# Optimization experiments

Hardware: AMD Instinct MI355X
Metric: run time of the kernel (lower is better)

## Reference

```python
import jax, jax.numpy as jnp
import numpy as np
import math

SPARSITY = 0.5
EPS = 1e-5


def _quant(x, bit, after_relu):
    # mirrors torch quantize_per_tensor math; straight-through (torch mutates x.data)
    def q(x):
        mx, mn = x.max(), x.min()
        scale = (mx - mn) / (2 ** bit - 1)
        if after_relu:
            ir = jnp.clip(jnp.round(x / scale), 0.0, 2 ** bit - 1)
            return ir * scale
        zp_min = jnp.floor(mn / scale)
        return (jnp.round((x - mn) / scale) + zp_min) * scale
    return x + jax.lax.stop_gradient(q(x) - x)


def _subnet(scores, k):
    # GetSubnet: top-k mask of |scores| with straight-through gradient
    s = jnp.abs(scores)
    flat = s.ravel()
    j = int((1.0 - k) * flat.size)
    order = jnp.argsort(flat)
    mask = jnp.zeros_like(flat).at[order[j:]].set(1.0).reshape(s.shape)
    return jax.lax.stop_gradient(mask - s) + s


def _scale(hw_one, fan_in):
    std = math.sqrt(2.0) / math.sqrt(fan_in * 0.5)
    return hw_one.mean() / std


def _blend_w(scores, sign, hw_one, hw_zero):
    m = _subnet(scores, SPARSITY)
    return sign * (hw_one[0] * m + hw_zero[0] * (1.0 - m))


def _conv(x, w):
    return jax.lax.conv_general_dilated(x, w, (1, 1), 'VALID',
                                        dimension_numbers=('NCHW', 'OIHW', 'NCHW'))


def _maxpool2(x):
    return jax.lax.reduce_window(x, -jnp.inf, jax.lax.max,
                                 (1, 1, 2, 2), (1, 1, 2, 2), 'VALID')


def _bn(x):
    m = x.mean((0, 2, 3), keepdims=True)
    v = x.var((0, 2, 3), keepdims=True)
    return (x - m) / jnp.sqrt(v + EPS)


def setup_inputs() -> dict:
    key = jax.random.key(0)
    ks = jax.random.split(key, 16)
    B = 4096
    shapes = {
        '1': (64, 1, 3, 3),
        '2': (16, 64, 3, 3),
        '3': (128, 400),
        '4': (10, 128),
    }
    inp = {'x': jax.random.normal(ks[0], (B, 1, 28, 28), dtype=jnp.float32)}
    i = 1
    for name, shp in shapes.items():
        inp['scores' + name] = jax.random.normal(ks[i], shp, dtype=jnp.float32); i += 1
        inp['sign' + name] = jnp.sign(jax.random.normal(ks[i], shp, dtype=jnp.float32)); i += 1
        inp['hw' + name + '_one'] = jax.random.uniform(ks[i], (1,) + shp, dtype=jnp.float32); i += 1
        # hw_zero: small "off" conductances
        inp['hw' + name + '_zero'] = 0.05 * jax.random.uniform(jax.random.fold_in(ks[i], 1), (1,) + shp, dtype=jnp.float32)
    inp['qb'] = 8
    return inp


def reference(x, scores1, sign1, hw1_one, hw1_zero,
              scores2, sign2, hw2_one, hw2_zero,
              scores3, sign3, hw3_one, hw3_zero,
              scores4, sign4, hw4_one, hw4_zero, qb):
    x = _maxpool2(x)
    x = _quant(x, qb, False)
    # conv1 (fan_in = 1*3*3 = 9)
    w1 = _blend_w(scores1, sign1, hw1_one, hw1_zero)
    x = _conv(x, w1) / _scale(hw1_one, 9)
    x = jax.nn.relu(_bn(x))
    x = _quant(x, qb, True)
    # conv2 (fan_in = 64*9 = 576)
    w2 = _blend_w(scores2, sign2, hw2_one, hw2_zero)
    x = _conv(x, w2) / _scale(hw2_one, 576)
    x = _maxpool2(x)
    x = jax.nn.relu(_bn(x))
    x = _quant(x, qb, True)
    x = x.reshape(x.shape[0], -1)  # [B, 400]
    # fc1 (fan_in = 400)
    w3 = _blend_w(scores3, sign3, hw3_one, hw3_zero)
    x = (x @ w3.T) / _scale(hw3_one, 400)
    x = jax.nn.relu(x)
    x = _quant(x, qb, True)
    # fc2 (fan_in = 128)
    w4 = _blend_w(scores4, sign4, hw4_one, hw4_zero)
    x = (x @ w4.T) / _scale(hw4_one, 128)
    return jax.nn.log_softmax(x, axis=1)
```

## Files before the change

### kernel.cpp

```cpp
#include <hip/hip_runtime.h>
#include <hip/hip_bf16.h>
#include <math.h>

#define DEV __device__ __forceinline__

constexpr int BATCH = 4096;
constexpr int NBA = 512;
constexpr int NBB = 512;
constexpr int NBC = 4096;
constexpr int NBE = 256;
constexpr int NBW = 16;

constexpr size_t OFF_POOLED = 0;
constexpr size_t OFF_Y2P = OFF_POOLED + (size_t)BATCH*196;
constexpr size_t OFF_ST1 = OFF_Y2P;
constexpr size_t OFF_H3  = OFF_Y2P + (size_t)BATCH*400;
constexpr size_t OFF_ST2 = OFF_H3;
constexpr size_t OFF_W2  = OFF_H3 + (size_t)BATCH*128;
constexpr size_t OFF_W3  = OFF_W2 + 9216;
constexpr size_t OFF_W4  = OFF_W3 + 51200;
constexpr size_t OFF_WSC = OFF_W4 + 1280;
constexpr size_t OFF_BN1 = OFF_WSC + 4;
constexpr size_t OFF_BN2 = OFF_BN1 + 256;
constexpr size_t OFF_GMM = OFF_BN2 + 64;
constexpr size_t OFF_ONS = OFF_GMM + 8;
constexpr size_t OFF_T   = OFF_ONS + 16;
constexpr size_t OFF_MMA = OFF_T + 4;
constexpr size_t OFF_HIST= OFF_MMA + 1024;
constexpr size_t OFF_W1M = OFF_HIST + 32768;
constexpr size_t OFF_SEL = OFF_W1M + 2048;
constexpr size_t OFF_H2G = OFF_SEL + 8;
constexpr size_t OFF_H3G = OFF_H2G + 4096;

typedef __attribute__((ext_vector_type(8))) short bf16x8;
typedef __attribute__((ext_vector_type(4))) float f32x4;

struct InPtrs {
  const float* x;
  const float* sc[4];
  const float* sg[4];
  const float* on[4];
  const float* ze[4];
  const int* qb;
};

__constant__ const int KW_L[16]  ={0,1,1,2,2,2,2,2,2,2,2,2,2,2,2,3};
__constant__ const int KW_S[16]  ={0,0,1,0,1,2,3,4,5,6,7,8,9,10,11,0};
__constant__ const int KW_NB[4]  ={1,2,12,1};
__constant__ const int KW_N[4]   ={576,9216,51200,1280};
__constant__ const int KW_FAN[4] ={9,576,400,128};
__constant__ const int KW_BW0[4] ={0,1,3,15};
__constant__ const int KW_BW1[4] ={1,3,15,16};

DEV unsigned fenc(float f){ unsigned u=__float_as_uint(f); return (u&0x80000000u)? ~u : (u|0x80000000u); }
DEV float fdec(unsigned e){ return __uint_as_float((e&0x80000000u)? (e&0x7fffffffu) : ~e); }
DEV unsigned short f2bf(float f){ unsigned u=__float_as_uint(f); return (unsigned short)((u + 0x7fffu + ((u>>16)&1u))>>16); }

DEV float blk_sum(float v, float* red, int t){
  red[t]=v; __syncthreads();
  for (int s=128;s>0;s>>=1){ if(t<s) red[t]+=red[t+s]; __syncthreads(); }
  float r=red[0]; __syncthreads();
  return r;
}
DEV float blk_min(float v, float* red, int t){
  red[t]=v; __syncthreads();
  for (int s=128;s>0;s>>=1){ if(t<s) red[t]=fminf(red[t],red[t+s]); __syncthreads(); }
  float r=red[0]; __syncthreads();
  return r;
}
DEV float blk_max(float v, float* red, int t){
  red[t]=v; __syncthreads();
  for (int s=128;s>0;s>>=1){ if(t<s) red[t]=fmaxf(red[t],red[t+s]); __syncthreads(); }
  float r=red[0]; __syncthreads();
  return r;
}

DEV int2 find256(const int* hist, int nbins, int kk, int t, int* suf, int* sh2){
  const int G=nbins>>8;
  const int lo=t*G;
  int g=0;
  for (int b=0;b<G;++b) g+=hist[lo+b];
  suf[t]=g; __syncthreads();
  for (int s=1;s<256;s<<=1){
    int add=(t+s<256)?suf[t+s]:0;
    __syncthreads();
    suf[t]+=add;
    __syncthreads();
  }
  const int S=suf[t];
  const int Snext=(t<255)?suf[t+1]:0;
  if (S>=kk && Snext<kk){
    int c2=Snext;
    for (int b=lo+G-1;b>=lo;--b){
      c2+=hist[b];
      if (c2>=kk){ sh2[0]=b; sh2[1]=kk-(c2-hist[b]); break; }
    }
  }
  __syncthreads();
  int2 r=make_int2(sh2[0],sh2[1]);
  __syncthreads();
  return r;
}

DEV void build_patq(unsigned* PATQ, const unsigned short* qxs, int t){
  for (int pos=t; pos<144; pos+=256){
    int py=(pos*171)>>11;
    int px=pos-py*12;
    const unsigned short* q0=qxs+py*16+px;
    unsigned e0=q0[0],  e1=q0[1],  e2=q0[2];
    unsigned e3=q0[16], e4=q0[17], e5=q0[18];
    unsigned e6=q0[32], e7=q0[33], e8=q0[34];
    *(uint4*)(PATQ+pos*4)      =make_uint4(e0|(e1<<16), e2|(e3<<16), e4|(e5<<16), e6|(e7<<16));
    *(uint4*)(PATQ+(144+pos)*4)=make_uint4(e8, 0u, 0u, 0u);
  }
}

__global__ __launch_bounds__(256) void ka_kernel(InPtrs in, float* __restrict__ ws){
  const int t=threadIdx.x, blk=blockIdx.x;
  __shared__ int h[2048];
  __shared__ float red[256];
  if (blk<NBA){
    if (blk==0){
      unsigned* Z=(unsigned*)(ws+OFF_H2G);
      for (int i=t;i<8192;i+=256) Z[i]=0u;
    }
    const float* x=in.x;
    float* pooled=ws+OFF_POOLED;
    float lmn=3.4e38f, lmx=-3.4e38f;
    if (t<196){
      const int oy=(t*2341)>>15;
      const int ox=t-oy*14;
      const float* xb=x+(size_t)blk*8*784+oy*56+ox*2;
      #pragma unroll
      for (int im=0; im<8; ++im){
        const float* px=xb+im*784;
        float m=fmaxf(fmaxf(px[0],px[1]),fmaxf(px[28],px[29]));
        pooled[(size_t)(blk*8+im)*196+t]=m;
        lmn=fminf(lmn,m); lmx=fmaxf(lmx,m);
      }
    }
    float bmn=blk_min(lmn,red,t);
    float bmx=blk_max(lmx,red,t);
    if (t==0){ ws[OFF_MMA+blk*2]=bmn; ws[OFF_MMA+blk*2+1]=bmx; }
  } else {
    const int bw=blk-NBA;
    const int L=KW_L[bw], s=KW_S[bw], nb=KW_NB[L];
    const int n4=KW_N[L]>>2;
    const int lo=(int)(((long long)n4*s)/nb), hi=(int)(((long long)n4*(s+1))/nb);
    const float4* sc4=(const float4*)in.sc[L];
    const float4* on4=(const float4*)in.on[L];
    for (int i=t;i<2048;i+=256) h[i]=0;
    __syncthreads();
    float onsum=0.f;
    for (int i=lo+t;i<hi;i+=256){
      float4 v=sc4[i];
      atomicAdd(&h[(__float_as_uint(v.x)&0x7fffffffu)>>20],1);
      atomicAdd(&h[(__float_as_uint(v.y)&0x7fffffffu)>>20],1);
      atomicAdd(&h[(__float_as_uint(v.z)&0x7fffffffu)>>20],1);
      atomicAdd(&h[(__float_as_uint(v.w)&0x7fffffffu)>>20],1);
      float4 o=on4[i];
      onsum+=(o.x+o.y)+(o.z+o.w);
    }
    __syncthreads();
    unsigned* GH=(unsigned*)(ws+OFF_HIST);
    for (int i=t;i<2048;i+=256) GH[bw*2048+i]=(unsigned)h[i];
    float S=blk_sum(onsum,red,t);
    if (t==0) ws[OFF_ONS+bw]=S;
  }
}

__global__ __launch_bounds__(256) void kwp2_kernel(InPtrs in, float* __restrict__ ws){
  const int t=threadIdx.x, bw=blockIdx.x;
  __shared__ int hist[2048];
  __shared__ int suf[256];
  __shared__ int sh2[2];
  __shared__ float redm[256], redx[256];
  const int L=KW_L[bw], s=KW_S[bw], nb=KW_NB[L];
  const int n4=KW_N[L]>>2;
  const int lo=(int)(((long long)n4*s)/nb), hi=(int)(((long long)n4*(s+1))/nb);
  if (bw==0){
    float a0=ws[OFF_MMA+2*t],       a1=ws[OFF_MMA+2*(t+256)];
    float b0v=ws[OFF_MMA+2*t+1],    b1v=ws[OFF_MMA+2*(t+256)+1];
    redm[t]=fminf(a0,a1); redx[t]=fmaxf(b0v,b1v);
    __syncthreads();
    for (int st=128;st>0;st>>=1){
      if (t<st){ redm[t]=fminf(redm[t],redm[t+st]); redx[t]=fmaxf(redx[t],redx[t+st]); }
      __syncthreads();
    }
    unsigned* U=(unsigned*)(ws+OFF_GMM);
    if (t==0){ U[0]=fenc(redm[0]); U[1]=fenc(redx[0]); }
    if (t>=2 && t<8) U[t]=(t&1)? 0u : 0xFFFFFFFFu;
    __syncthreads();
  }
  if (bw==15){
    unsigned* z=(unsigned*)(ws+OFF_W1M);
    for (int i=t;i<2048;i+=256) z[i]=0u;
  }
  const unsigned* GH=(const unsigned*)(ws+OFF_HIST);
  for (int i=t;i<2048;i+=256){
    int sm=0;
    for (int b2=KW_BW0[L]; b2<KW_BW1[L]; ++b2) sm+=(int)GH[b2*2048+i];
    hist[i]=sm;
  }
  __syncthreads();
  int2 f1=find256(hist,2048,KW_N[L]>>1,t,suf,sh2);
  const unsigned b0=(unsigned)f1.x;
  if (s==0 && t==0){
    unsigned* SEL=(unsigned*)(ws+OFF_SEL);
    SEL[L*2]=(unsigned)f1.x; SEL[L*2+1]=(unsigned)f1.y;
  }
  const float4* sc4=(const float4*)in.sc[L];
  unsigned* GH2=(unsigned*)(ws+OFF_H2G)+L*1024;
  for (int i=lo+t;i<hi;i+=256){
    float4 v=sc4[i];
    unsigned ux=__float_as_uint(v.x)&0x7fffffffu;
    unsigned uy=__float_as_uint(v.y)&0x7fffffffu;
    unsigned uz=__float_as_uint(v.z)&0x7fffffffu;
    unsigned uw=__float_as_uint(v.w)&0x7fffffffu;
    if ((ux>>20)==b0) atomicAdd(&GH2[(ux>>10)&1023u],1u);
    if ((uy>>20)==b0) atomicAdd(&GH2[(uy>>10)&1023u],1u);
    if ((uz>>20)==b0) atomicAdd(&GH2[(uz>>10)&1023u],1u);
    if ((uw>>20)==b0) atomicAdd(&GH2[(uw>>10)&1023u],1u);
  }
}

__global__ __launch_bounds__(256) void kwp3_kernel(InPtrs in, float* __restrict__ ws){
  const int t=threadIdx.x, bw=blockIdx.x;
  const int L=KW_L[bw], s=KW_S[bw], nb=KW_NB[L];
  const int n4=KW_N[L]>>2;
  const int lo=(int)(((long long)n4*s)/nb), hi=(int)(((long long)n4*(s+1))/nb);
  const unsigned* SEL=(const unsigned*)(ws+OFF_SEL);
  const unsigned b0=SEL[L*2]; const int r1=(int)SEL[L*2+1];
  __shared__ int hist[1024];
  __shared__ int suf[256];
  __shared__ int sh2[2];
  const unsigned* GH2=(const unsigned*)(ws+OFF_H2G)+L*1024;
  for (int i=t;i<1024;i+=256) hist[i]=(int)GH2[i];
  __syncthreads();
  int2 f2=find256(hist,1024,r1,t,suf,sh2);
  const unsigned pre=(b0<<10)|(unsigned)f2.x;
  const float4* sc4=(const float4*)in.sc[L];
  unsigned* GH3=(unsigned*)(ws+OFF_H3G)+L*1024;
  for (int i=lo+t;i<hi;i+=256){
    float4 v=sc4[i];
    unsigned ux=__float_as_uint(v.x)&0x7fffffffu;
    unsigned uy=__float_as_uint(v.y)&0x7fffffffu;
    unsigned uz=__float_as_uint(v.z)&0x7fffffffu;
    unsigned uw=__float_as_uint(v.w)&0x7fffffffu;
    if ((ux>>10)==pre) atomicAdd(&GH3[ux&1023u],1u);
    if ((uy>>10)==pre) atomicAdd(&GH3[uy&1023u],1u);
    if ((uz>>10)==pre) atomicAdd(&GH3[uz&1023u],1u);
    if ((uw>>10)==pre) atomicAdd(&GH3[uw&1023u],1u);
  }
}

__global__ __launch_bounds__(256) void kw3_kernel(InPtrs in, float* __restrict__ ws){
  const int t=threadIdx.x, bw=blockIdx.x;
  const int L=KW_L[bw], s=KW_S[bw], nb=KW_NB[L];
  const int n4=KW_N[L]>>2;
  const int lo=(int)(((long long)n4*s)/nb), hi=(int)(((long long)n4*(s+1))/nb);
  const unsigned* SEL=(const unsigned*)(ws+OFF_SEL);
  const unsigned b0=SEL[L*2]; const int r1=(int)SEL[L*2+1];
  __shared__ int hist[1024];
  __shared__ int suf[256];
  __shared__ int sh2[2];
  const unsigned* GH2=(const unsigned*)(ws+OFF_H2G)+L*1024;
  for (int i=t;i<1024;i+=256) hist[i]=(int)GH2[i];
  __syncthreads();
  int2 f2=find256(hist,1024,r1,t,suf,sh2);
  const unsigned pre=(b0<<10)|(unsigned)f2.x;
  const int r2=f2.y;
  __syncthreads();
  const unsigned* GH3=(const unsigned*)(ws+OFF_H3G)+L*1024;
  for (int i=t;i<1024;i+=256) hist[i]=(int)GH3[i];
  __syncthreads();
  int2 f3=find256(hist,1024,r2,t,suf,sh2);
  const unsigned T=(pre<<10)|(unsigned)f3.x;
  if (s==0 && t==0){
    float os=0.f;
    for (int b=KW_BW0[L]; b<KW_BW1[L]; ++b) os+=ws[OFF_ONS+b];
    ws[OFF_WSC+L]=(os/(float)KW_N[L])*sqrtf((float)KW_FAN[L])*0.5f;
  }
  const float4* sc4=(const float4*)in.sc[L];
  const float4* sg4=(const float4*)in.sg[L];
  const float4* on4=(const float4*)in.on[L];
  const float4* ze4=(const float4*)in.ze[L];
  float* wout=ws+OFF_W4;
  unsigned* W3Fu=(unsigned*)(ws+OFF_W3);
  unsigned short* W1F=(unsigned short*)(ws+OFF_W1M);
  unsigned short* W2F=(unsigned short*)(ws+OFF_W2);
  for (int i4=lo+t;i4<hi;i4+=256){
    float4 sv4=sc4[i4], g=sg4[i4], o=on4[i4], z=ze4[i4];
    float sv[4]={sv4.x,sv4.y,sv4.z,sv4.w}, gv[4]={g.x,g.y,g.z,g.w};
    float ov[4]={o.x,o.y,o.z,o.w}, zv[4]={z.x,z.y,z.z,z.w};
    #pragma unroll
    for (int j=0;j<4;++j){
      int i=i4*4+j;
      unsigned u=__float_as_uint(sv[j])&0x7fffffffu;
      float w=gv[j]*((u>=T)? ov[j] : zv[j]);
      if (L==0){
        int oc=i/9; int k=i-oc*9;
        int ocT=oc>>4, ocL=oc&15, quad=k>>3, kj=k&7;
        unsigned short hb=f2bf(w);
        float lo2=w-__uint_as_float((unsigned)hb<<16);
        W1F[((((ocT*2+0)*4+quad)*16+ocL)<<3)+kj]=hb;
        W1F[((((ocT*2+1)*4+quad)*16+ocL)<<3)+kj]=f2bf(lo2);
      } else if (L==1){
        int oc=i/576; int r=i-oc*576; int ic=r/9; int kp=r-ic*9;
        int ss=ic>>5, rem=ic&31, quad=rem>>3, kj=rem&7;
        unsigned short hb=f2bf(w);
        float lo2=w-__uint_as_float((unsigned)hb<<16);
        W2F[(((((kp*2+ss)*2+0)*4+quad)*16+oc)<<3)+kj]=hb;
        W2F[(((((kp*2+ss)*2+1)*4+quad)*16+oc)<<3)+kj]=f2bf(lo2);
      } else if (L==2){
        int oc=i/400; int kk=i-oc*400;
        unsigned short hb=f2bf(w);
        float lo2=w-__uint_as_float((unsigned)hb<<16);
        unsigned short lb=f2bf(lo2);
        int ct=oc>>4, l15=oc&15;
        unsigned idx=((unsigned)((kk>>4)*8+ct)*64u + (unsigned)(((kk>>2)&3)*16+l15))*4u + (unsigned)(kk&3);
        W3Fu[idx]=(unsigned)hb | ((unsigned)lb<<16);
      } else {
        wout[i]=w;
      }
    }
  }
}

__global__ __launch_bounds__(256) void kb_kernel(InPtrs in, const float* __restrict__ wsr, float* __restrict__ wsw){
  const int t=threadIdx.x, blk=blockIdx.x;
  __shared__ unsigned short qxs[256];
  __shared__ __align__(16) unsigned PAT[2304];
  __shared__ float xw[1024];
  const float* pooled=wsr+OFF_POOLED;
  const unsigned* U=(const unsigned*)(wsr+OFF_GMM);
  const float mn0=fdec(U[0]);
  const float mx0=fdec(U[1]);
  const float lvf=(float)((1<<in.qb[0])-1);
  const float s0=(mx0-mn0)/lvf, inv_s0=1.0f/s0, zp0=floorf(mn0/s0);
  const float sv=s0/wsr[OFF_WSC+0];
  const int w=t>>6, lane=t&63, l15=lane&15, quad=lane>>4;
  const unsigned short* W1F=(const unsigned short*)(wsr+OFF_W1M);
  bf16x8 bh[4], bl[4];
  #pragma unroll
  for (int ocT=0; ocT<4; ++ocT){
    bh[ocT]=*(const bf16x8*)(W1F+(((ocT*2+0)*64+lane)<<3));
    bl[ocT]=*(const bf16x8*)(W1F+(((ocT*2+1)*64+lane)<<3));
  }
  for (int i=1152+t; i<2304; i+=256) PAT[i]=0u;
  float sum[4], sq[4], mn[4], mx[4];
  #pragma unroll
  for (int i=0;i<4;++i){ sum[i]=0.f; sq[i]=0.f; mn[i]=3.4e38f; mx[i]=-3.4e38f; }
  for (int img=0; img<8; ++img){
    if (t<224){
      int row=t>>4, col=t&15;
      float q=0.f;
      if (col<14){ float xx=pooled[(size_t)(blk*8+img)*196+row*14+col]; q=rintf((xx-mn0)*inv_s0)+zp0; }
      qxs[t]=(unsigned short)(__float_as_uint(q)>>16);
    }
    __syncthreads();
    build_patq(PAT,qxs,t);
    __syncthreads();
    const unsigned short* PATu=(const unsigned short*)PAT;
    #pragma unroll
    for (int ocT=0; ocT<4; ++ocT){
      for (int tl=w; tl<9; tl+=4){
        bf16x8 a=*(const bf16x8*)(PATu+((quad*144+tl*16+l15)<<3));
        f32x4 acc=(f32x4){0.f,0.f,0.f,0.f};
        acc=__builtin_amdgcn_mfma_f32_16x16x32_bf16(a,bh[ocT],acc,0,0,0);
        acc=__builtin_amdgcn_mfma_f32_16x16x32_bf16(a,bl[ocT],acc,0,0,0);
        #pragma unroll
        for (int r=0;r<4;++r){
          float v=acc[r];
          sum[ocT]+=v; sq[ocT]=fmaf(v,v,sq[ocT]);
          mn[ocT]=fminf(mn[ocT],v); mx[ocT]=fmaxf(mx[ocT],v);
        }
      }
    }
    __syncthreads();
  }
  #pragma unroll
  for (int ocT=0; ocT<4; ++ocT){
    float s=sum[ocT], q2=sq[ocT], a=mn[ocT], b=mx[ocT];
    #pragma unroll
    for (int d=16;d<64;d<<=1){
      s+=__shfl_xor(s,d);
      q2+=__shfl_xor(q2,d);
      a=fminf(a,__shfl_xor(a,d));
      b=fmaxf(b,__shfl_xor(b,d));
    }
    if (quad==0){
      float* p=xw+((w*4+ocT)*16+l15)*4;
      p[0]=s; p[1]=q2; p[2]=a; p[3]=b;
    }
  }
  __syncthreads();
  if (t<64){
    float s=0.f,q2=0.f,a=3.4e38f,b=-3.4e38f;
    #pragma unroll
    for (int w2=0;w2<4;++w2){
      const float* p=xw+((w2*4+(t>>4))*16+(t&15))*4;
      s+=p[0]; q2+=p[1]; a=fminf(a,p[2]); b=fmaxf(b,p[3]);
    }
    float* p=wsw+OFF_ST1+((size_t)t*NBB+blk)*4;
    p[0]=s*sv; p[1]=q2*sv*sv; p[2]=a*sv; p[3]=b*sv;
  }
}

__global__ __launch_bounds__(256) void kstat_kernel(const float* __restrict__ wsr, float* __restrict__ wsw,
                                                    unsigned long long inoff, int nparts, float Nf,
                                                    unsigned long long outoff, int mmslot){
  const int c=blockIdx.x, t=threadIdx.x;
  __shared__ float red[256];
  const float* p=wsr+inoff+(size_t)c*nparts*4;
  float sum=0.f,sq=0.f,mn=3.4e38f,mx=-3.4e38f;
  for (int i=t;i<nparts;i+=256){
    sum+=p[i*4]; sq+=p[i*4+1];
    mn=fminf(mn,p[i*4+2]); mx=fmaxf(mx,p[i*4+3]);
  }
  float S=blk_sum(sum,red,t);
  float Q=blk_sum(sq,red,t);
  float MN=blk_min(mn,red,t);
  float MX=blk_max(mx,red,t);
  if (t==0){
    float mean=S/Nf;
    float var=fmaxf(Q/Nf-mean*mean,0.f);
    float sd=sqrtf(var+1e-5f);
    float* o=wsw+outoff+c*4;
    float tmn=(MN-mean)/sd, tmx=(MX-mean)/sd;
    o[0]=mean; o[1]=sd; o[2]=tmn; o[3]=tmx;
    unsigned* U=(unsigned*)(wsw+OFF_GMM);
    atomicMin(&U[mmslot],fenc(tmn));
    atomicMax(&U[mmslot+1],fenc(tmx));
  }
}

__global__ __launch_bounds__(256) void kc_kernel(InPtrs in, const float* __restrict__ wsr, float* __restrict__ wsw){
  const int t=threadIdx.x, blk=blockIdx.x;
  __shared__ unsigned short qxs[256];
  __shared__ __align__(16) unsigned PATBUF[3328];
  __shared__ __align__(16) unsigned short actA[144*88];
  __shared__ float sA2[64], sB2[64];
  unsigned* PAT=PATBUF;
  float (*c2sP)[16][104]=(float(*)[16][104])PATBUF;
  const float* pooled=wsr+OFF_POOLED;
  const unsigned* U=(const unsigned*)(wsr+OFF_GMM);
  const float mn0=fdec(U[0]);
  const float mx0=fdec(U[1]);
  const float rmn=fdec(U[2]);
  const float rmx=fdec(U[3]);
  const float lvf=(float)((1<<in.qb[0])-1);
  const float s0=(mx0-mn0)/lvf, inv_s0=1.0f/s0, zp0=floorf(mn0/s0);
  const float s1w=wsr[OFF_WSC+0], s2w=wsr[OFF_WSC+1];
  const float s2=(fmaxf(rmx,0.f)-fmaxf(rmn,0.f))/lvf;
  const float inv_s2=1.0f/s2;
  const float g2=s2/s2w;
  if (t<64){
    float m=wsr[OFF_BN1+t*4], sd=wsr[OFF_BN1+t*4+1];
    sA2[t]=s0/(s1w*sd)*inv_s2;
    sB2[t]=(-m/sd)*inv_s2;
  }
  if (t<224){
    int row=t>>4, col=t&15;
    float q=0.f;
    if (col<14){ float xx=pooled[(size_t)blk*196+row*14+col]; q=rintf((xx-mn0)*inv_s0)+zp0; }
    qxs[t]=(unsigned short)(__float_as_uint(q)>>16);
  }
  for (int i=1152+t; i<2304; i+=256) PAT[i]=0u;
  __syncthreads();
  build_patq(PAT,qxs,t);
  __syncthreads();
  const int w=t>>6, lane=t&63;
  const int l15=lane&15, quad=lane>>4;
  {
    const unsigned short* W1F=(const unsigned short*)(wsr+OFF_W1M);
    const unsigned short* PATu=(const unsigned short*)PAT;
    #pragma unroll
    for (int ocT=0; ocT<4; ++ocT){
      bf16x8 bh=*(const bf16x8*)(W1F+(((ocT*2+0)*64+lane)<<3));
      bf16x8 bl=*(const bf16x8*)(W1F+(((ocT*2+1)*64+lane)<<3));
      const int oc0=ocT*16+quad*4;
      const float a20=sA2[oc0],   b20=sB2[oc0];
      const float a21=sA2[oc0+1], b21=sB2[oc0+1];
      const float a22=sA2[oc0+2], b22=sB2[oc0+2];
      const float a23=sA2[oc0+3], b23=sB2[oc0+3];
      for (int tl=w; tl<9; tl+=4){
        bf16x8 a=*(const bf16x8*)(PATu+((quad*144+tl*16+l15)<<3));
        f32x4 acc=(f32x4){0.f,0.f,0.f,0.f};
        acc=__builtin_amdgcn_mfma_f32_16x16x32_bf16(bh,a,acc,0,0,0);
        acc=__builtin_amdgcn_mfma_f32_16x16x32_bf16(bl,a,acc,0,0,0);
        const int pos=tl*16+l15;
        float f0=fminf(rintf(fmaxf(fmaf(acc[0],a20,b20),0.f)),lvf);
        float f1=fminf(rintf(fmaxf(fmaf(acc[1],a21,b21),0.f)),lvf);
        float f2v=fminf(rintf(fmaxf(fmaf(acc[2],a22,b22),0.f)),lvf);
        float f3=fminf(rintf(fmaxf(fmaf(acc[3],a23,b23),0.f)),lvf);
        unsigned w0=(__float_as_uint(f0)>>16)|((__float_as_uint(f1)>>16)<<16);
        unsigned w1=(__float_as_uint(f2v)>>16)|((__float_as_uint(f3)>>16)<<16);
        *(uint2*)(actA+pos*88+oc0)=make_uint2(w0,w1);
      }
    }
  }
  __syncthreads();
  {
    const int wm=w>>1, wk=w&1;
    const int k0=wk?5:0, nK=wk?4:5;
    const int nT2=wm?3:4;
    const unsigned short* W2F=(const unsigned short*)(wsr+OFF_W2);
    int abase[4];
    #pragma unroll
    for (int i=0;i<4;++i){
      int tau=wm*4+i;
      int posb=tau*16+l15;
      int pc=posb>99?99:posb;
      int py=pc/10, px=pc-py*10;
      abase[i]=(py*12+px)*176+quad*16;
    }
    f32x4 acc[4];
    acc[0]=(f32x4){0.f,0.f,0.f,0.f};
    acc[1]=(f32x4){0.f,0.f,0.f,0.f};
    acc[2]=(f32x4){0.f,0.f,0.f,0.f};
    acc[3]=(f32x4){0.f,0.f,0.f,0.f};
    const char* actB=(const char*)actA;
    #pragma unroll
    for (int kk=0;kk<5;++kk){
      if (kk<nK){
        int kykx=k0+kk;
        int ky=(kykx*11)>>5;
        int kx=kykx-ky*3;
        int co=(ky*12+kx)*176;
        #pragma unroll
        for (int s=0;s<2;++s){
          bf16x8 bh=*(const bf16x8*)(W2F+((((kykx*2+s)*2+0)*64+lane)<<3));
          bf16x8 bl=*(const bf16x8*)(W2F+((((kykx*2+s)*2+1)*64+lane)<<3));
          #pragma unroll
          for (int i=0;i<4;++i){
            if (i<nT2){
              bf16x8 a=*(const bf16x8*)(actB+abase[i]+co+s*64);
              acc[i]=__builtin_amdgcn_mfma_f32_16x16x32_bf16(a,bh,acc[i],0,0,0);
              acc[i]=__builtin_amdgcn_mfma_f32_16x16x32_bf16(a,bl,acc[i],0,0,0);
            }
          }
        }
      }
    }
    #pragma unroll
    for (int i=0;i<4;++i){
      if (i<nT2){
        int pos4=(wm*4+i)*16+quad*4;
        if (pos4<100){
          float4* dst=(float4*)&c2sP[wk][l15][pos4];
          *dst=make_float4(acc[i].x*g2,acc[i].y*g2,acc[i].z*g2,acc[i].w*g2);
        }
      }
    }
  }
  __syncthreads();
  {
    const int ch=t>>4, g=t&15;
    const float* cc0=&c2sP[0][ch][0];
    const float* cc1=&c2sP[1][ch][0];
    float sum=0.f,sq=0.f,mn=3.4e38f,mx=-3.4e38f;
    #pragma unroll
    for (int it=0;it<2;++it){
      int j=g+it*16;
      if (j<25){
        int py=(j*52)>>8;
        int px=j-py*5;
        int base=py*20+px*2;
        float2 p0=*(const float2*)(cc0+base);
        float2 p1=*(const float2*)(cc0+base+10);
        float2 q0=*(const float2*)(cc1+base);
        float2 q1=*(const float2*)(cc1+base+10);
        float a0=p0.x+q0.x, a1=p0.y+q0.y;
        float b0=p1.x+q1.x, b1=p1.y+q1.y;
        float v=fmaxf(fmaxf(a0,a1),fmaxf(b0,b1));
        wsw[OFF_Y2P+(size_t)blk*400+ch*25+j]=v;
        sum+=v; sq=fmaf(v,v,sq); mn=fminf(mn,v); mx=fmaxf(mx,v);
      }
    }
    #pragma unroll
    for (int d=1;d<16;d<<=1){
      sum+=__shfl_xor(sum,d);
      sq +=__shfl_xor(sq,d);
      mn=fminf(mn,__shfl_xor(mn,d));
      mx=fmaxf(mx,__shfl_xor(mx,d));
    }
    if (g==0){
      float* p=wsw+OFF_ST2+((size_t)ch*NBC+blk)*4;
      p[0]=sum; p[1]=sq; p[2]=mn; p[3]=mx;
    }
  }
}

__global__ __launch_bounds__(512) void ke_kernel(InPtrs in, const float* __restrict__ wsr, float* __restrict__ wsw){
  const int t=threadIdx.x, blk=blockIdx.x;
  __shared__ __align__(16) unsigned short xs[16*808];
  __shared__ float sm[16], sisd[16];
  __shared__ float rwn[8], rwx[8];
  const unsigned* U=(const unsigned*)(wsr+OFF_GMM);
  const float lvf=(float)((1<<in.qb[0])-1);
  const float rmn=fdec(U[4]);
  const float rmx=fdec(U[5]);
  if (t<16){ sm[t]=wsr[OFF_BN2+t*4]; sisd[t]=1.0f/wsr[OFF_BN2+t*4+1]; }
  const float s3=(fmaxf(rmx,0.f)-fmaxf(rmn,0.f))/lvf;
  const float inv_s3=1.0f/s3;
  const float inv_s3w=1.0f/wsr[OFF_WSC+2];
  const int b0=blk*16;
  __syncthreads();
  {
    const int img=t>>5, tg=t&31;
    const float* yrow=wsr+OFF_Y2P+(size_t)(b0+img)*400;
    unsigned* xsu=(unsigned*)xs;
    for (int n=0;n<13;++n){
      int k=n*32+tg;
      if (k<400){
        int ch=(k*5243)>>17;
        float y=yrow[k];
        float r=fmaxf((y-sm[ch])*sisd[ch],0.f);
        float q=fminf(rintf(r*inv_s3),lvf);
        unsigned qb=__float_as_uint(q)>>16;
        xsu[img*404+k]=qb|(qb<<16);
      }
    }
  }
  __syncthreads();
  const int w=t>>6, lane=t&63, l15=lane&15, quad=lane>>4;
  const int ct=w;
  const bf16x8* Wf=(const bf16x8*)(wsr+OFF_W3);
  const unsigned short* arow=xs+l15*808;
  f32x4 acc=(f32x4){0.f,0.f,0.f,0.f};
  #pragma unroll 5
  for (int kt=0;kt<25;++kt){
    bf16x8 a=*(const bf16x8*)(arow+kt*32+quad*8);
    bf16x8 b=Wf[(kt*8+ct)*64+lane];
    acc=__builtin_amdgcn_mfma_f32_16x16x32_bf16(a,b,acc,0,0,0);
  }
  const float scale=s3*inv_s3w;
  float hmn=3.4e38f,hmx=-3.4e38f;
  #pragma unroll
  for (int r=0;r<4;++r){
    float h=fmaxf(acc[r]*scale,0.f);
    wsw[OFF_H3+(size_t)(b0+quad*4+r)*128+ct*16+l15]=h;
    hmn=fminf(hmn,h); hmx=fmaxf(hmx,h);
  }
  #pragma unroll
  for (int d=1;d<64;d<<=1){
    hmn=fminf(hmn,__shfl_xor(hmn,d));
    hmx=fmaxf(hmx,__shfl_xor(hmx,d));
  }
  if (lane==0){ rwn[w]=hmn; rwx[w]=hmx; }
  __syncthreads();
  if (t==0){
    float mn=rwn[0], mx=rwx[0];
    #pragma unroll
    for (int i=1;i<8;++i){ mn=fminf(mn,rwn[i]); mx=fmaxf(mx,rwx[i]); }
    float* p=wsw+OFF_MMA+(size_t)blk*2;
    p[0]=mn; p[1]=mx;
  }
}

__global__ __launch_bounds__(256) void kf_kernel(InPtrs in, const float* __restrict__ wsr, float* __restrict__ out){
  const int t=threadIdx.x, blk=blockIdx.x;
  __shared__ float w4s[1280];
  __shared__ float redn[256], redxs[256];
  const float lvf=(float)((1<<in.qb[0])-1);
  for (int i=t;i<1280;i+=256) w4s[i]=wsr[OFF_W4+i];
  {
    const float* mmp=wsr+OFF_MMA;
    float mn=3.4e38f, mx=-3.4e38f;
    if (t<NBE){
      mn=mmp[2*t];
      mx=mmp[2*t+1];
    }
    redn[t]=mn; redxs[t]=mx;
    __syncthreads();
    for (int s=128;s>0;s>>=1){
      if (t<s){ redn[t]=fminf(redn[t],redn[t+s]); redxs[t]=fmaxf(redxs[t],redxs[t+s]); }
      __syncthreads();
    }
  }
  const float hmn=redn[0];
  const float hmx=redxs[0];
  const float s4=(hmx-hmn)/lvf;
  const float inv_s4=1.0f/s4;
  const float inv_s4w=1.0f/wsr[OFF_WSC+3];
  const int row=blk*64+(t>>2), l4=t&3;
  const float4* hr4=(const float4*)(wsr+OFF_H3+(size_t)row*128);
  float acc[10];
  #pragma unroll
  for (int j=0;j<10;++j) acc[j]=0.f;
  #pragma unroll 2
  for (int j=0;j<8;++j){
    float4 v=hr4[l4*8+j];
    int kb=(l4*8+j)*4;
    float q0=fminf(rintf(v.x*inv_s4),lvf)*s4;
    float q1=fminf(rintf(v.y*inv_s4),lvf)*s4;
    float q2=fminf(rintf(v.z*inv_s4),lvf)*s4;
    float q3=fminf(rintf(v.w*inv_s4),lvf)*s4;
    #pragma unroll
    for (int o=0;o<10;++o){
      const float* wr=w4s+o*128+kb;
      acc[o]=fmaf(q0,wr[0],acc[o]);
      acc[o]=fmaf(q1,wr[1],acc[o]);
      acc[o]=fmaf(q2,wr[2],acc[o]);
      acc[o]=fmaf(q3,wr[3],acc[o]);
    }
  }
  #pragma unroll
  for (int o=0;o<10;++o){
    acc[o]+=__shfl_xor(acc[o],1);
    acc[o]+=__shfl_xor(acc[o],2);
  }
  if (l4==0){
    float mx=-3.4e38f;
    #pragma unroll
    for (int o=0;o<10;++o){ acc[o]*=inv_s4w; mx=fmaxf(mx,acc[o]); }
    float se=0.f;
    #pragma unroll
    for (int o=0;o<10;++o) se+=expf(acc[o]-mx);
    const float ls=logf(se);
    #pragma unroll
    for (int o=0;o<10;++o) out[row*10+o]=acc[o]-mx-ls;
  }
}

extern "C" void kernel_launch(void* const* d_in, const int* in_sizes, int n_in,
                              void* d_out, int out_size, void* d_ws, size_t ws_size,
                              hipStream_t stream){
  (void)in_sizes; (void)n_in; (void)out_size; (void)ws_size;
  InPtrs P;
  P.x=(const float*)d_in[0];
  for (int l=0;l<4;++l){
    P.sc[l]=(const float*)d_in[1+l*4];
    P.sg[l]=(const float*)d_in[2+l*4];
    P.on[l]=(const float*)d_in[3+l*4];
    P.ze[l]=(const float*)d_in[4+l*4];
  }
  P.qb=(const int*)d_in[17];
  float* ws=(float*)d_ws;

  hipLaunchKernelGGL(ka_kernel,   dim3(NBA+NBW), dim3(256), 0, stream, P, ws);
  hipLaunchKernelGGL(kwp2_kernel, dim3(NBW),     dim3(256), 0, stream, P, ws);
  hipLaunchKernelGGL(kwp3_kernel, dim3(NBW),     dim3(256), 0, stream, P, ws);
  hipLaunchKernelGGL(kw3_kernel,  dim3(NBW),     dim3(256), 0, stream, P, ws);
  hipLaunchKernelGGL(kb_kernel,   dim3(NBB),     dim3(256), 0, stream, P, ws, ws);
  hipLaunchKernelGGL(kstat_kernel, dim3(64), dim3(256), 0, stream, ws, ws,
                     (unsigned long long)OFF_ST1, NBB, 4096.f*144.f, (unsigned long long)OFF_BN1, 2);
  hipLaunchKernelGGL(kc_kernel,   dim3(NBC),     dim3(256), 0, stream, P, ws, ws);
  hipLaunchKernelGGL(kstat_kernel, dim3(16), dim3(256), 0, stream, ws, ws,
                     (unsigned long long)OFF_ST2, NBC, 4096.f*25.f, (unsigned long long)OFF_BN2, 4);
  hipLaunchKernelGGL(ke_kernel,   dim3(NBE),     dim3(512), 0, stream, P, ws, ws);
  hipLaunchKernelGGL(kf_kernel,   dim3(64),      dim3(256), 0, stream, P, ws, (float*)d_out);
}
```

Measured before the change: 232.4 us.

## Split conv2 MFMA work by position tiles instead of K-split across warps

The conv2 MFMA stage was previously split across warps by both position tile and kernel-tap range, with two partial-sum planes reduced in the pooling stage. Now each warp owns whole position tiles and loops over all 9 taps, which drops the extra partial buffer and the add during pooling. The activation row stride shrinks from 88 to 72, and the shared buffers shrink with it, which may raise occupancy but could add LDS bank conflicts. An extra barrier is added because the output buffer now aliases the pattern buffer, and warp loads become uneven (2 vs 1 tiles).

```diff
diff --git a/kernel.cpp b/kernel.cpp
--- a/kernel.cpp
+++ b/kernel.cpp
@@ -438,11 +438,11 @@
 __global__ __launch_bounds__(256) void kc_kernel(InPtrs in, const float* __restrict__ wsr, float* __restrict__ wsw){
   const int t=threadIdx.x, blk=blockIdx.x;
   __shared__ unsigned short qxs[256];
-  __shared__ __align__(16) unsigned PATBUF[3328];
-  __shared__ __align__(16) unsigned short actA[144*88];
+  __shared__ __align__(16) unsigned PATBUF[2304];
+  __shared__ __align__(16) unsigned short actA[144*72];
   __shared__ float sA2[64], sB2[64];
   unsigned* PAT=PATBUF;
-  float (*c2sP)[16][104]=(float(*)[16][104])PATBUF;
+  float (*c2s)[100]=(float(*)[100])PATBUF;
   const float* pooled=wsr+OFF_POOLED;
   const unsigned* U=(const unsigned*)(wsr+OFF_GMM);
   const float mn0=fdec(U[0]);
@@ -496,59 +496,53 @@
         float f3=fminf(rintf(fmaxf(fmaf(acc[3],a23,b23),0.f)),lvf);
         unsigned w0=(__float_as_uint(f0)>>16)|((__float_as_uint(f1)>>16)<<16);
         unsigned w1=(__float_as_uint(f2v)>>16)|((__float_as_uint(f3)>>16)<<16);
-        *(uint2*)(actA+pos*88+oc0)=make_uint2(w0,w1);
+        *(uint2*)(actA+pos*72+oc0)=make_uint2(w0,w1);
       }
     }
   }
   __syncthreads();
   {
-    const int wm=w>>1, wk=w&1;
-    const int k0=wk?5:0, nK=wk?4:5;
-    const int nT2=wm?3:4;
+    const int nT=(w<3)?2:1;
     const unsigned short* W2F=(const unsigned short*)(wsr+OFF_W2);
-    int abase[4];
-    #pragma unroll
-    for (int i=0;i<4;++i){
-      int tau=wm*4+i;
+    int abase[2];
+    #pragma unroll
+    for (int i=0;i<2;++i){
+      int tau=w+i*4;
       int posb=tau*16+l15;
       int pc=posb>99?99:posb;
       int py=pc/10, px=pc-py*10;
-      abase[i]=(py*12+px)*176+quad*16;
-    }
-    f32x4 acc[4];
+      abase[i]=(py*12+px)*144+quad*16;
+    }
+    f32x4 acc[2];
     acc[0]=(f32x4){0.f,0.f,0.f,0.f};
     acc[1]=(f32x4){0.f,0.f,0.f,0.f};
-    acc[2]=(f32x4){0.f,0.f,0.f,0.f};
-    acc[3]=(f32x4){0.f,0.f,0.f,0.f};
     const char* actB=(const char*)actA;
-    #pragma unroll
-    for (int kk=0;kk<5;++kk){
-      if (kk<nK){
-        int kykx=k0+kk;
-        int ky=(kykx*11)>>5;
-        int kx=kykx-ky*3;
-        int co=(ky*12+kx)*176;
+    #pragma unroll 3
+    for (int kykx=0;kykx<9;++kykx){
+      int ky=(kykx*11)>>5;
+      int kx=kykx-ky*3;
+      int co=(ky*12+kx)*144;
+      #pragma unroll
+      for (int s=0;s<2;++s){
+        bf16x8 bh=*(const bf16x8*)(W2F+((((kykx*2+s)*2+0)*64+lane)<<3));
+        bf16x8 bl=*(const bf16x8*)(W2F+((((kykx*2+s)*2+1)*64+lane)<<3));
         #pragma unroll
-        for (int s=0;s<2;++s){
-          bf16x8 bh=*(const bf16x8*)(W2F+((((kykx*2+s)*2+0)*64+lane)<<3));
-          bf16x8 bl=*(const bf16x8*)(W2F+((((kykx*2+s)*2+1)*64+lane)<<3));
-          #pragma unroll
-          for (int i=0;i<4;++i){
-            if (i<nT2){
-              bf16x8 a=*(const bf16x8*)(actB+abase[i]+co+s*64);
-              acc[i]=__builtin_amdgcn_mfma_f32_16x16x32_bf16(a,bh,acc[i],0,0,0);
-              acc[i]=__builtin_amdgcn_mfma_f32_16x16x32_bf16(a,bl,acc[i],0,0,0);
-            }
+        for (int i=0;i<2;++i){
+          if (i<nT){
+            bf16x8 a=*(const bf16x8*)(actB+abase[i]+co+s*64);
+            acc[i]=__builtin_amdgcn_mfma_f32_16x16x32_bf16(a,bh,acc[i],0,0,0);
+            acc[i]=__builtin_amdgcn_mfma_f32_16x16x32_bf16(a,bl,acc[i],0,0,0);
           }
         }
       }
     }
-    #pragma unroll
-    for (int i=0;i<4;++i){
-      if (i<nT2){
-        int pos4=(wm*4+i)*16+quad*4;
+    __syncthreads();
+    #pragma unroll
+    for (int i=0;i<2;++i){
+      if (i<nT){
+        int pos4=(w+i*4)*16+quad*4;
         if (pos4<100){
-          float4* dst=(float4*)&c2sP[wk][l15][pos4];
+          float4* dst=(float4*)&c2s[l15][pos4];
           *dst=make_float4(acc[i].x*g2,acc[i].y*g2,acc[i].z*g2,acc[i].w*g2);
         }
       }
@@ -557,8 +551,7 @@
   __syncthreads();
   {
     const int ch=t>>4, g=t&15;
-    const float* cc0=&c2sP[0][ch][0];
-    const float* cc1=&c2sP[1][ch][0];
+    const float* cc=&c2s[ch][0];
     float sum=0.f,sq=0.f,mn=3.4e38f,mx=-3.4e38f;
     #pragma unroll
     for (int it=0;it<2;++it){
@@ -567,13 +560,9 @@
         int py=(j*52)>>8;
         int px=j-py*5;
         int base=py*20+px*2;
-        float2 p0=*(const float2*)(cc0+base);
-        float2 p1=*(const float2*)(cc0+base+10);
-        float2 q0=*(const float2*)(cc1+base);
-        float2 q1=*(const float2*)(cc1+base+10);
-        float a0=p0.x+q0.x, a1=p0.y+q0.y;
-        float b0=p1.x+q1.x, b1=p1.y+q1.y;
-        float v=fmaxf(fmaxf(a0,a1),fmaxf(b0,b1));
+        float2 p0=*(const float2*)(cc+base);
+        float2 p1=*(const float2*)(cc+base+10);
+        float v=fmaxf(fmaxf(p0.x,p0.y),fmaxf(p1.x,p1.y));
         wsw[OFF_Y2P+(size_t)blk*400+ch*25+j]=v;
         sum+=v; sq=fmaf(v,v,sq); mn=fminf(mn,v); mx=fmaxf(mx,v);
       }
```

After: 230.9 us. About the same (-0.7%).
